# Optimization experiments

Measured on AMD Instinct MI355X. Metric: run time of the kernel, lower is better.

Reference implementation:

```python
import jax, jax.numpy as jnp
import numpy as np

LONG, LAT = 256, 256
N = LONG * LAT
BATCH = 64
OUT_DIM = 16 * 16


def _build_coo():
    # Faithful reproduction of the torch init loops (vectorized):
    # identity diagonal + 8-neighbor stencil entries for interior rows,
    # each (x,y) pair added in BOTH (x,y) and (y,x) directions.
    # torch sparse matmul on the uncoalesced COO sums duplicate entries,
    # so shared interior edges effectively get weight 2 -- the .at[].add
    # scatter below reproduces exactly that summation semantics.
    diag = np.arange(N, dtype=np.int64)
    centers = np.arange(LAT + 1, (LONG - 1) * LAT - 1, dtype=np.int64)
    offs = np.array([-1, 1, LAT, -LAT, LAT - 1, LAT + 1, -LAT - 1, -LAT + 1], dtype=np.int64)
    neigh = (centers[:, None] + offs[None, :]).ravel()
    crep = np.repeat(centers, 8)
    rows = np.concatenate([diag, crep, neigh]).astype(np.int32)
    cols = np.concatenate([diag, neigh, crep]).astype(np.int32)
    vals = np.ones(rows.shape[0], dtype=np.float32)
    return rows, cols, vals


def setup_inputs() -> dict:
    key = jax.random.key(0)
    k1, k2, k3 = jax.random.split(key, 3)
    rows, cols, vals = _build_coo()
    x = jax.random.normal(k1, (BATCH, LONG, LAT), dtype=jnp.float32)
    W = jax.random.normal(k2, (OUT_DIM, N), dtype=jnp.float32) * 0.02  # lin1.weight
    b = jax.random.normal(k3, (OUT_DIM,), dtype=jnp.float32) * 0.02   # lin1.bias
    return {
        "x": x,
        "W": W,
        "b": b,
        "rows": jnp.asarray(rows),
        "cols": jnp.asarray(cols),
        "vals": jnp.asarray(vals),
    }


def reference(x, W, b, rows, cols, vals):
    B = x.shape[0]
    xf = x.reshape(B, -1)                      # [B, N]
    gathered = xf[:, cols] * vals               # [B, E]
    h1 = jnp.zeros((B, xf.shape[1]), xf.dtype).at[:, rows].add(gathered)  # A @ xf.T, transposed
    h2 = h1 @ W.T + b                           # dense linear
    return h2
```

## Files before the change

kernel.cpp:

```cpp
#include <hip/hip_runtime.h>
#include <hip/hip_bf16.h>


#define MB     64
#define NOUT   256
#define KDIM   65536
#define NTOT   (MB * KDIM)
#define KP     2048
#define NKP    (KDIM / KP)
#define OTOT   (MB * NOUT)

typedef __attribute__((ext_vector_type(8))) short bf16x8;
typedef __attribute__((ext_vector_type(8))) unsigned short ushort8v;
typedef __attribute__((ext_vector_type(4))) float f32x4;

__device__ __forceinline__ ushort f2bf(float f) {
    __hip_bfloat16 h = __float2bfloat16(f);
    return *reinterpret_cast<ushort*>(&h);
}

__global__ __launch_bounds__(256) void stencil_bf16(const float* __restrict__ x,
                                                    ushort* __restrict__ h1) {
    const int g  = (blockIdx.x * 256 + threadIdx.x) * 8;
    const int i8 = g & (KDIM - 1);
    union Span { float4 v[4]; float f[16]; };
    Span u, c, d;
    #pragma unroll
    for (int q = 0; q < 4; ++q) {
        int bu = g - 260 + 4 * q; if (bu < 0) bu = 0;
        int bc = g - 4   + 4 * q; if (bc < 0) bc = 0; if (bc > NTOT - 4) bc = NTOT - 4;
        int bd = g + 252 + 4 * q; if (bd > NTOT - 4) bd = NTOT - 4;
        u.v[q] = *(const float4*)(x + bu);
        c.v[q] = *(const float4*)(x + bc);
        d.v[q] = *(const float4*)(x + bd);
    }
    ushort8v ov;
    if (i8 >= 520 && i8 <= 65008) {
        #pragma unroll
        for (int e = 0; e < 8; ++e) {
            float nb = c.f[3 + e] + c.f[5 + e]
                     + u.f[3 + e] + u.f[4 + e] + u.f[5 + e]
                     + d.f[3 + e] + d.f[4 + e] + d.f[5 + e];
            ov[e] = (short)f2bf(fmaf(2.0f, nb, c.f[4 + e]));
        }
    } else {
        #pragma unroll
        for (int e = 0; e < 8; ++e) {
            const int ii = i8 + e;
            const float ci = ((unsigned)(ii - 257) <= (65278u - 257u)) ? 1.0f : 0.0f;
            float s = c.f[4 + e];
            const int   doff[8] = {-1, 1, -257, -256, -255, 255, 256, 257};
            const float* src[8] = {&c.f[3 + e], &c.f[5 + e],
                                   &u.f[3 + e], &u.f[4 + e], &u.f[5 + e],
                                   &d.f[3 + e], &d.f[4 + e], &d.f[5 + e]};
            #pragma unroll
            for (int t = 0; t < 8; ++t) {
                const int j = ii + doff[t];
                const float cj = ((unsigned)(j - 257) <= (65278u - 257u)) ? 1.0f : 0.0f;
                s = fmaf(ci + cj, *src[t], s);
            }
            ov[e] = (short)f2bf(s);
        }
    }
    *(ushort8v*)(h1 + g) = ov;
}

__global__ __launch_bounds__(1024, 4) void gemm_mfma(const ushort* __restrict__ h1,
                                                     const float* __restrict__ W,
                                                     float* __restrict__ part) {
    __shared__ float red[16 * 1024];
    const int d   = blockIdx.x;
    const int xcd = d & 7;
    const int idx = d >> 3;
    const int nt  = idx & 15;
    const int kp  = xcd + 8 * (idx >> 4);
    const int wv = threadIdx.x >> 6;
    const int l  = threadIdx.x & 63;
    const int lr = l & 15;
    const int lg = l >> 4;
    const size_t kb = (size_t)kp * KP + wv * 128 + lg * 8;

    f32x4 acc[4];
    #pragma unroll
    for (int a = 0; a < 4; ++a) acc[a] = (f32x4){0.f, 0.f, 0.f, 0.f};

    const ushort* ap = h1 + (size_t)lr * KDIM + kb;
    const float*  wp = W + (size_t)(nt * 16 + lr) * KDIM + kb;

    #pragma unroll
    for (int ks = 0; ks < 4; ++ks) {
        bf16x8 afrag[4];
        #pragma unroll
        for (int mt = 0; mt < 4; ++mt)
            afrag[mt] = *(const bf16x8*)(ap + (size_t)mt * 16 * KDIM + ks * 32);
        float4 w0 = *(const float4*)(wp + ks * 32);
        float4 w1 = *(const float4*)(wp + ks * 32 + 4);
        union { ushort u[8]; bf16x8 v; } bb;
        bb.u[0] = f2bf(w0.x); bb.u[1] = f2bf(w0.y);
        bb.u[2] = f2bf(w0.z); bb.u[3] = f2bf(w0.w);
        bb.u[4] = f2bf(w1.x); bb.u[5] = f2bf(w1.y);
        bb.u[6] = f2bf(w1.z); bb.u[7] = f2bf(w1.w);
        #pragma unroll
        for (int mt = 0; mt < 4; ++mt)
            acc[mt] = __builtin_amdgcn_mfma_f32_16x16x32_bf16(afrag[mt], bb.v,
                                                              acc[mt], 0, 0, 0);
    }

    #pragma unroll
    for (int mt = 0; mt < 4; ++mt)
        #pragma unroll
        for (int r = 0; r < 4; ++r)
            red[wv * 1024 + (mt * 16 + lg * 4 + r) * 16 + lr] = acc[mt][r];
    __syncthreads();

    const int t = threadIdx.x;
    float s0 = 0.f, s1 = 0.f;
    #pragma unroll
    for (int j = 0; j < 16; j += 2) {
        s0 += red[j * 1024 + t];
        s1 += red[(j + 1) * 1024 + t];
    }
    part[(size_t)kp * OTOT + (t >> 4) * NOUT + nt * 16 + (t & 15)] = s0 + s1;
}

__global__ __launch_bounds__(256) void reduce_f32(const float* __restrict__ part,
                                                  const float* __restrict__ bias,
                                                  float* __restrict__ out) {
    __shared__ float red[256];
    const int ol = threadIdx.x & 31;
    const int cg = threadIdx.x >> 5;
    const int o  = blockIdx.x * 32 + ol;
    const float* p = part + (size_t)cg * 4 * OTOT + o;
    red[threadIdx.x] = (p[0] + p[OTOT]) + (p[2 * OTOT] + p[3 * OTOT]);
    __syncthreads();
    if (cg == 0) {
        float v = red[ol];
        #pragma unroll
        for (int jj = 1; jj < 8; ++jj) v += red[jj * 32 + ol];
        out[o] = v + bias[o & (NOUT - 1)];
    }
}

extern "C" void kernel_launch(void* const* d_in, const int* in_sizes, int n_in,
                              void* d_out, int out_size, void* d_ws, size_t ws_size,
                              hipStream_t stream) {
    const float* x    = (const float*)d_in[0];
    const float* W    = (const float*)d_in[1];
    const float* bias = (const float*)d_in[2];
    float* out = (float*)d_out;

    ushort* h1b  = (ushort*)d_ws;
    float*  part = (float*)((char*)d_ws + (size_t)MB * KDIM * 2);

    stencil_bf16<<<NTOT / (256 * 8), 256, 0, stream>>>(x, h1b);
    gemm_mfma<<<16 * NKP, 1024, 0, stream>>>(h1b, W, part);
    reduce_f32<<<OTOT / 32, 256, 0, stream>>>(part, bias, out);
}
```

Baseline: 40.82 us.

## Restructure GEMM split-K: per-wave M tiles, longer K loop, drop LDS reduction

The GEMM kernel moves from 1024-thread blocks, where 16 waves each handled a K slice for all four M tiles and were combined through a large LDS reduction, to 256-thread blocks. Each wave now owns one M tile and loops over the whole K partition, whose size is halved to 1024, so there are twice as many blocks. Partial results are written directly as f32x4 in a transposed layout, and the reduce kernel sums 64 partitions and transposes back on output. This removes the LDS traffic and the barrier, but each W tile is now reloaded by four waves, and the partial buffer and reduce work double.

After: 62.74 us. 53.7% more time.

```diff
diff --git a/kernel.cpp b/kernel.cpp
--- a/kernel.cpp
+++ b/kernel.cpp
@@ -6,7 +6,7 @@
 #define NOUT   256
 #define KDIM   65536
 #define NTOT   (MB * KDIM)
-#define KP     2048
+#define KP     1024
 #define NKP    (KDIM / KP)
 #define OTOT   (MB * NOUT)
 
@@ -19,9 +19,8 @@
     return *reinterpret_cast<ushort*>(&h);
 }
 
-__global__ __launch_bounds__(256) void stencil_bf16(const float* __restrict__ x,
-                                                    ushort* __restrict__ h1) {
-    const int g  = (blockIdx.x * 256 + threadIdx.x) * 8;
+__device__ __forceinline__ void stencil8(const float* __restrict__ x,
+                                         ushort* __restrict__ h1, int g) {
     const int i8 = g & (KDIM - 1);
     union Span { float4 v[4]; float f[16]; };
     Span u, c, d;
@@ -65,34 +64,34 @@
     *(ushort8v*)(h1 + g) = ov;
 }
 
-__global__ __launch_bounds__(1024, 4) void gemm_mfma(const ushort* __restrict__ h1,
-                                                     const float* __restrict__ W,
-                                                     float* __restrict__ part) {
-    __shared__ float red[16 * 1024];
+__global__ __launch_bounds__(256) void stencil_bf16(const float* __restrict__ x,
+                                                    ushort* __restrict__ h1) {
+    const int g = (blockIdx.x * 256 + threadIdx.x) * 8;
+    stencil8(x, h1, g);
+}
+
+__global__ __launch_bounds__(256, 4) void gemm_mfma(const ushort* __restrict__ h1,
+                                                    const float* __restrict__ W,
+                                                    float* __restrict__ part) {
     const int d   = blockIdx.x;
     const int xcd = d & 7;
     const int idx = d >> 3;
     const int nt  = idx & 15;
     const int kp  = xcd + 8 * (idx >> 4);
-    const int wv = threadIdx.x >> 6;
-    const int l  = threadIdx.x & 63;
-    const int lr = l & 15;
-    const int lg = l >> 4;
-    const size_t kb = (size_t)kp * KP + wv * 128 + lg * 8;
+    const int mt  = threadIdx.x >> 6;
+    const int l   = threadIdx.x & 63;
+    const int lr  = l & 15;
+    const int lg  = l >> 4;
+    const size_t kb = (size_t)kp * KP + lg * 8;
 
-    f32x4 acc[4];
-    #pragma unroll
-    for (int a = 0; a < 4; ++a) acc[a] = (f32x4){0.f, 0.f, 0.f, 0.f};
+    f32x4 acc = (f32x4){0.f, 0.f, 0.f, 0.f};
 
-    const ushort* ap = h1 + (size_t)lr * KDIM + kb;
+    const ushort* ap = h1 + (size_t)(mt * 16 + lr) * KDIM + kb;
     const float*  wp = W + (size_t)(nt * 16 + lr) * KDIM + kb;
 
-    #pragma unroll
-    for (int ks = 0; ks < 4; ++ks) {
-        bf16x8 afrag[4];
-        #pragma unroll
-        for (int mt = 0; mt < 4; ++mt)
-            afrag[mt] = *(const bf16x8*)(ap + (size_t)mt * 16 * KDIM + ks * 32);
+    #pragma unroll 8
+    for (int ks = 0; ks < KP / 32; ++ks) {
+        bf16x8 afrag = *(const bf16x8*)(ap + ks * 32);
         float4 w0 = *(const float4*)(wp + ks * 32);
         float4 w1 = *(const float4*)(wp + ks * 32 + 4);
         union { ushort u[8]; bf16x8 v; } bb;
@@ -100,27 +99,12 @@
         bb.u[2] = f2bf(w0.z); bb.u[3] = f2bf(w0.w);
         bb.u[4] = f2bf(w1.x); bb.u[5] = f2bf(w1.y);
         bb.u[6] = f2bf(w1.z); bb.u[7] = f2bf(w1.w);
-        #pragma unroll
-        for (int mt = 0; mt < 4; ++mt)
-            acc[mt] = __builtin_amdgcn_mfma_f32_16x16x32_bf16(afrag[mt], bb.v,
-                                                              acc[mt], 0, 0, 0);
+        acc = __builtin_amdgcn_mfma_f32_16x16x32_bf16(afrag, bb.v, acc, 0, 0, 0);
     }
 
-    #pragma unroll
-    for (int mt = 0; mt < 4; ++mt)
-        #pragma unroll
-        for (int r = 0; r < 4; ++r)
-            red[wv * 1024 + (mt * 16 + lg * 4 + r) * 16 + lr] = acc[mt][r];
-    __syncthreads();
-
-    const int t = threadIdx.x;
-    float s0 = 0.f, s1 = 0.f;
-    #pragma unroll
-    for (int j = 0; j < 16; j += 2) {
-        s0 += red[j * 1024 + t];
-        s1 += red[(j + 1) * 1024 + t];
-    }
-    part[(size_t)kp * OTOT + (t >> 4) * NOUT + nt * 16 + (t & 15)] = s0 + s1;
+    float* pb = part + (size_t)kp * OTOT + (size_t)(nt * 16 + lr) * MB
+              + mt * 16 + lg * 4;
+    *(f32x4*)pb = acc;
 }
 
 __global__ __launch_bounds__(256) void reduce_f32(const float* __restrict__ part,
@@ -130,14 +114,23 @@
     const int ol = threadIdx.x & 31;
     const int cg = threadIdx.x >> 5;
     const int o  = blockIdx.x * 32 + ol;
-    const float* p = part + (size_t)cg * 4 * OTOT + o;
-    red[threadIdx.x] = (p[0] + p[OTOT]) + (p[2 * OTOT] + p[3 * OTOT]);
+    const float* p = part + (size_t)cg * 8 * OTOT + o;
+    float s0 = 0.f, s1 = 0.f, s2 = 0.f, s3 = 0.f;
+    #pragma unroll
+    for (int i = 0; i < 8; i += 4) {
+        s0 += p[(size_t)(i + 0) * OTOT];
+        s1 += p[(size_t)(i + 1) * OTOT];
+        s2 += p[(size_t)(i + 2) * OTOT];
+        s3 += p[(size_t)(i + 3) * OTOT];
+    }
+    red[threadIdx.x] = (s0 + s1) + (s2 + s3);
     __syncthreads();
     if (cg == 0) {
         float v = red[ol];
         #pragma unroll
         for (int jj = 1; jj < 8; ++jj) v += red[jj * 32 + ol];
-        out[o] = v + bias[o & (NOUT - 1)];
+        const int n = o >> 6, m = o & 63;
+        out[m * NOUT + n] = v + bias[n];
     }
 }
 
@@ -153,6 +146,6 @@
     float*  part = (float*)((char*)d_ws + (size_t)MB * KDIM * 2);
 
     stencil_bf16<<<NTOT / (256 * 8), 256, 0, stream>>>(x, h1b);
-    gemm_mfma<<<16 * NKP, 1024, 0, stream>>>(h1b, W, part);
+    gemm_mfma<<<16 * NKP, 256, 0, stream>>>(h1b, W, part);
     reduce_f32<<<OTOT / 32, 256, 0, stream>>>(part, bias, out);
 }
```
